# Kernel optimization log

Measured on AMD Instinct MI355X. Metric: run time of the kernel, lower is better.

Reference implementation:

```python
import jax, jax.numpy as jnp
import numpy as np

V = 33279   # num_tokens
E = 256     # embedding_size
H = 512     # hidden_size
NH = 8      # num_heads
L = 4       # num_layers
DH = E // NH
MAXPOS = 64


def _ln(x, g, b):
    mu = jnp.mean(x, axis=-1, keepdims=True)
    var = jnp.mean((x - mu) ** 2, axis=-1, keepdims=True)
    return (x - mu) / jnp.sqrt(var + 1e-5) * g + b


def setup_inputs() -> dict:
    key = jax.random.key(0)
    ks = jax.random.split(key, 32)
    N, S = 128, 64
    label = jax.random.randint(ks[0], (N, S), 0, V)
    # Bernoulli(0.15) BERT-style mask (deterministic stand-in for torch sampling)
    mask = (jax.random.uniform(ks[1], (N, S)) < 0.15).astype(jnp.int32)
    s = 0.02
    inp = {
        'label': label, 'mask': mask,
        'emb': jax.random.normal(ks[2], (V + 1, E)) * s,
        'pos': jax.random.normal(ks[3], (MAXPOS, E)) * s,
        'emb_g': jnp.ones((E,)), 'emb_b': jnp.zeros((E,)),
        # stacked per-layer params (leading dim L)
        'Wq': jax.random.normal(ks[4], (L, E, E)) * s, 'bq': jnp.zeros((L, E)),
        'Wk': jax.random.normal(ks[5], (L, E, E)) * s, 'bk': jnp.zeros((L, E)),
        'Wv': jax.random.normal(ks[6], (L, E, E)) * s, 'bv': jnp.zeros((L, E)),
        'Wo': jax.random.normal(ks[7], (L, E, E)) * s, 'bo': jnp.zeros((L, E)),
        'n1g': jnp.ones((L, E)), 'n1b': jnp.zeros((L, E)),
        'W1': jax.random.normal(ks[8], (L, E, H)) * s, 'b1': jnp.zeros((L, H)),
        'W2': jax.random.normal(ks[9], (L, H, E)) * s, 'b2': jnp.zeros((L, E)),
        'n2g': jnp.ones((L, E)), 'n2b': jnp.zeros((L, E)),
        # decoder head
        'dW1': jax.random.normal(ks[10], (E, E)) * s, 'db1': jnp.zeros((E,)),
        'dng': jnp.ones((E,)), 'dnb': jnp.zeros((E,)),
        'dW2': jax.random.normal(ks[11], (E, V)) * s, 'db2': jnp.zeros((V,)),
    }
    return inp


def reference(label, mask, emb, pos, emb_g, emb_b, Wq, bq, Wk, bk, Wv, bv,
              Wo, bo, n1g, n1b, W1, b1, W2, b2, n2g, n2b,
              dW1, db1, dng, dnb, dW2, db2):
    N, S = label.shape
    src_ids = jnp.where(mask == 1, V, label)  # masked-token id = num_tokens
    # embedding + positional, then LayerNorm (eval: Scaler/Dropout identity)
    x = emb[src_ids] + pos[:S][None, :, :]
    x = _ln(x, emb_g, emb_b)
    temp = jnp.asarray((E // NH) ** 0.5, x.dtype)

    def layer(x, p):
        wq, bq_, wk, bk_, wv, bv_, wo, bo_, g1, b1n, w1, b1_, w2, b2_, g2, b2n = p
        q = (x @ wq + bq_).reshape(N, S, NH, DH).transpose(0, 2, 1, 3)
        k = (x @ wk + bk_).reshape(N, S, NH, DH).transpose(0, 2, 1, 3)
        v = (x @ wv + bv_).reshape(N, S, NH, DH).transpose(0, 2, 1, 3)
        scores = jnp.einsum('nhsd,nhtd->nhst', q, k) / temp
        attn = jax.nn.softmax(scores, axis=-1)
        o = jnp.einsum('nhst,nhtd->nhsd', attn, v)
        o = o.transpose(0, 2, 1, 3).reshape(N, S, E) @ wo + bo_
        x1 = _ln(x + o, g1, b1n)
        ff = jax.nn.gelu(x1 @ w1 + b1_, approximate=False) @ w2 + b2_
        x2 = _ln(x1 + ff, g2, b2n)
        return x2, None

    x, _ = jax.lax.scan(layer, x, (Wq, bq, Wk, bk, Wv, bv, Wo, bo,
                                   n1g, n1b, W1, b1, W2, b2, n2g, n2b))
    # decoder head: linear -> gelu -> LN -> vocab projection
    h = jax.nn.gelu(x @ dW1 + db1, approximate=False)
    h = _ln(h, dng, dnb)
    logits = h @ dW2 + db2               # [N, S, V]
    logp = jax.nn.log_softmax(logits, axis=-1)
    loss = -jnp.take_along_axis(logp, label[..., None], axis=-1).mean()
    score = logits.transpose(0, 2, 1)    # [N, V, S] like torch permute(0,2,1)
    return score, loss
```

## Files before the change

### kernel.cpp

```cpp
#include <hip/hip_runtime.h>
#include <hip/hip_bf16.h>

#define DEVFN static __device__ __forceinline__

constexpr int N_ = 128, S_ = 64, T_ = N_ * S_;
constexpr int E_ = 256, H_ = 512, NH_ = 8, DH_ = 32, L_ = 4;
constexpr int V_ = 33279, VPAD_ = 33280, NVT_ = VPAD_ / 128;

typedef __attribute__((ext_vector_type(8))) short bf16x8;
typedef __attribute__((ext_vector_type(4))) float f32x4;
typedef unsigned short ushort_t;

DEVFN ushort_t f2bf(float f) {
  unsigned int u = __float_as_uint(f);
  unsigned int r = (u + 0x7fffu + ((u >> 16) & 1u)) >> 16;
  return (ushort_t)r;
}
DEVFN float bf2f(ushort_t u) { return __uint_as_float(((unsigned)u) << 16); }

DEVFN float geluf(float x) {
  return 0.5f * x * (1.f + erff(x * 0.70710678118654752440f));
}

DEVFN float wave_sum(float v) {
  #pragma unroll
  for (int off = 32; off >= 1; off >>= 1) v += __shfl_xor(v, off, 64);
  return v;
}

__global__ __launch_bounds__(256) void k_embed_ln(
    const int* __restrict__ label, const int* __restrict__ mask,
    const float* __restrict__ emb, const float* __restrict__ pos,
    const float* __restrict__ g, const float* __restrict__ b,
    float* __restrict__ x, ushort_t* __restrict__ xb) {
  int wv = threadIdx.x >> 6, lane = threadIdx.x & 63;
  int t = blockIdx.x * 4 + wv;
  int s = t & (S_ - 1);
  int id = (mask[t] == 1) ? V_ : label[t];
  int c = lane * 4;
  float4 v = *(const float4*)&emb[(size_t)id * E_ + c];
  float4 p = *(const float4*)&pos[s * E_ + c];
  v.x += p.x; v.y += p.y; v.z += p.z; v.w += p.w;
  float mean = wave_sum(v.x + v.y + v.z + v.w) * (1.f / E_);
  float4 d = {v.x - mean, v.y - mean, v.z - mean, v.w - mean};
  float var = wave_sum(d.x * d.x + d.y * d.y + d.z * d.z + d.w * d.w) * (1.f / E_);
  float rstd = 1.f / sqrtf(var + 1e-5f);
  float4 g4 = *(const float4*)&g[c];
  float4 b4 = *(const float4*)&b[c];
  float4 y = {d.x * rstd * g4.x + b4.x, d.y * rstd * g4.y + b4.y,
              d.z * rstd * g4.z + b4.z, d.w * rstd * g4.w + b4.w};
  *(float4*)&x[(size_t)t * E_ + c] = y;
  ushort4 yb = {f2bf(y.x), f2bf(y.y), f2bf(y.z), f2bf(y.w)};
  *(ushort4*)&xb[(size_t)t * E_ + c] = yb;
}

__global__ __launch_bounds__(256) void k_add_ln(
    const float* __restrict__ a, const float* __restrict__ bsrc,
    const float* __restrict__ g, const float* __restrict__ bet,
    float* __restrict__ y, ushort_t* __restrict__ yb) {
  int wv = threadIdx.x >> 6, lane = threadIdx.x & 63;
  int t = blockIdx.x * 4 + wv;
  int c = lane * 4;
  float4 v = *(const float4*)&a[(size_t)t * E_ + c];
  if (bsrc) {
    float4 u = *(const float4*)&bsrc[(size_t)t * E_ + c];
    v.x += u.x; v.y += u.y; v.z += u.z; v.w += u.w;
  }
  float mean = wave_sum(v.x + v.y + v.z + v.w) * (1.f / E_);
  float4 d = {v.x - mean, v.y - mean, v.z - mean, v.w - mean};
  float var = wave_sum(d.x * d.x + d.y * d.y + d.z * d.z + d.w * d.w) * (1.f / E_);
  float rstd = 1.f / sqrtf(var + 1e-5f);
  float4 g4 = *(const float4*)&g[c];
  float4 b4 = *(const float4*)&bet[c];
  float4 o = {d.x * rstd * g4.x + b4.x, d.y * rstd * g4.y + b4.y,
              d.z * rstd * g4.z + b4.z, d.w * rstd * g4.w + b4.w};
  if (y) *(float4*)&y[(size_t)t * E_ + c] = o;
  if (yb) {
    ushort4 ob = {f2bf(o.x), f2bf(o.y), f2bf(o.z), f2bf(o.w)};
    *(ushort4*)&yb[(size_t)t * E_ + c] = ob;
  }
}

__global__ __launch_bounds__(256) void k_bcat(
    const float* __restrict__ bq, const float* __restrict__ bk,
    const float* __restrict__ bv, float* __restrict__ bqkv) {
  int l = blockIdx.x, i = threadIdx.x;
  bqkv[l * 768 + i]       = bq[l * 256 + i];
  bqkv[l * 768 + 256 + i] = bk[l * 256 + i];
  bqkv[l * 768 + 512 + i] = bv[l * 256 + i];
}

__global__ __launch_bounds__(256) void k_wt(const float* __restrict__ src,
                                            ushort_t* __restrict__ dst,
                                            int K, int J, int dstLayerStride) {
  __shared__ float tile[32][33];
  int j0 = blockIdx.x * 32, k0 = blockIdx.y * 32, l = blockIdx.z;
  src += (size_t)l * K * J;
  dst += (size_t)l * dstLayerStride;
  int tx = threadIdx.x & 31, ty = threadIdx.x >> 5;
  #pragma unroll
  for (int rr = 0; rr < 4; rr++) {
    int kk = ty * 4 + rr;
    tile[kk][tx] = src[(size_t)(k0 + kk) * J + j0 + tx];
  }
  __syncthreads();
  #pragma unroll
  for (int rr = 0; rr < 4; rr++) {
    int jj = ty * 4 + rr;
    dst[(size_t)(j0 + jj) * K + k0 + tx] = f2bf(tile[tx][jj]);
  }
}

template <int K, int OUT_BF16, int GELU_>
__global__ __launch_bounds__(256) void k_mm(
    const ushort_t* __restrict__ Xb, const ushort_t* __restrict__ WT,
    const float* __restrict__ bias, void* __restrict__ C, int Nout) {
  constexpr int STR = K + 8;
  __shared__ ushort_t xs[64 * STR];
  int tid = threadIdx.x, lane = tid & 63, wv = tid >> 6;
  int t0 = blockIdx.x * 64, j0 = blockIdx.y * 64;
  const ushort_t* xsrc = Xb + (size_t)t0 * K;
  for (int i = tid; i < 64 * (K / 8); i += 256) {
    int r = i / (K / 8), c = (i % (K / 8)) * 8;
    *(uint4*)&xs[r * STR + c] = *(const uint4*)&xsrc[(size_t)r * K + c];
  }
  __syncthreads();
  int l15 = lane & 15, l4 = lane >> 4;
  f32x4 acc[4] = {};
  const ushort_t* xrow = &xs[(wv * 16 + l15) * STR + l4 * 8];
  const ushort_t* wrow = WT + (size_t)j0 * K + l4 * 8;
  #pragma unroll
  for (int kb = 0; kb < K / 32; kb++) {
    bf16x8 a = *(const bf16x8*)(xrow + kb * 32);
    #pragma unroll
    for (int st = 0; st < 4; st++) {
      bf16x8 bfr = *(const bf16x8*)(wrow + (size_t)(st * 16 + l15) * K + kb * 32);
      acc[st] = __builtin_amdgcn_mfma_f32_16x16x32_bf16(a, bfr, acc[st], 0, 0, 0);
    }
  }
  #pragma unroll
  for (int st = 0; st < 4; st++) {
    int j = j0 + st * 16 + l15;
    float bv_ = bias[j];
    #pragma unroll
    for (int r = 0; r < 4; r++) {
      float val = acc[st][r] + bv_;
      if (GELU_) val = geluf(val);
      int t = t0 + wv * 16 + l4 * 4 + r;
      if (OUT_BF16)
        ((ushort_t*)C)[(size_t)t * Nout + j] = f2bf(val);
      else
        ((float*)C)[(size_t)t * Nout + j] = val;
    }
  }
}

__global__ __launch_bounds__(256) void k_attn(
    const ushort_t* __restrict__ qkv, ushort_t* __restrict__ o) {
  __shared__ __align__(16) ushort_t vt_[32 * 72];
  __shared__ __align__(16) ushort_t ps[64 * 72];
  int n = blockIdx.x >> 3, h = blockIdx.x & 7;
  int tid = threadIdx.x, lane = tid & 63, wv = tid >> 6;
  int l15 = lane & 15, l4 = lane >> 4;
  const ushort_t* qbase = qkv + (size_t)n * S_ * 768 + h * DH_;
  for (int i = tid; i < S_ * DH_; i += 256) {
    int t = i >> 5, d = i & 31;
    vt_[d * 72 + t] = qbase[(size_t)t * 768 + 512 + d];
  }
  int srow = wv * 16 + l15;
  bf16x8 aq = *(const bf16x8*)&qbase[(size_t)srow * 768 + l4 * 8];
  f32x4 sc[4];
  #pragma unroll
  for (int st = 0; st < 4; st++) {
    bf16x8 bk_ = *(const bf16x8*)&qbase[(size_t)(st * 16 + l15) * 768 + 256 + l4 * 8];
    f32x4 z = {};
    sc[st] = __builtin_amdgcn_mfma_f32_16x16x32_bf16(aq, bk_, z, 0, 0, 0);
  }
  const float scale = 0.17677669529663687f;
  #pragma unroll
  for (int st = 0; st < 4; st++)
    #pragma unroll
    for (int r = 0; r < 4; r++) sc[st][r] *= scale;
  #pragma unroll
  for (int r = 0; r < 4; r++) {
    float m = fmaxf(fmaxf(sc[0][r], sc[1][r]), fmaxf(sc[2][r], sc[3][r]));
    m = fmaxf(m, __shfl_xor(m, 1, 64));
    m = fmaxf(m, __shfl_xor(m, 2, 64));
    m = fmaxf(m, __shfl_xor(m, 4, 64));
    m = fmaxf(m, __shfl_xor(m, 8, 64));
    float p0 = __expf(sc[0][r] - m), p1 = __expf(sc[1][r] - m);
    float p2 = __expf(sc[2][r] - m), p3 = __expf(sc[3][r] - m);
    float sum = p0 + p1 + p2 + p3;
    sum += __shfl_xor(sum, 1, 64);
    sum += __shfl_xor(sum, 2, 64);
    sum += __shfl_xor(sum, 4, 64);
    sum += __shfl_xor(sum, 8, 64);
    float inv = 1.f / sum;
    int prow = (wv * 16 + l4 * 4 + r) * 72;
    ps[prow + 0 * 16 + l15] = f2bf(p0 * inv);
    ps[prow + 1 * 16 + l15] = f2bf(p1 * inv);
    ps[prow + 2 * 16 + l15] = f2bf(p2 * inv);
    ps[prow + 3 * 16 + l15] = f2bf(p3 * inv);
  }
  __syncthreads();
  f32x4 oc[2] = {};
  #pragma unroll
  for (int kb = 0; kb < 2; kb++) {
    bf16x8 ap = *(const bf16x8*)&ps[srow * 72 + kb * 32 + l4 * 8];
    #pragma unroll
    for (int st2 = 0; st2 < 2; st2++) {
      bf16x8 bv_ = *(const bf16x8*)&vt_[(st2 * 16 + l15) * 72 + kb * 32 + l4 * 8];
      oc[st2] = __builtin_amdgcn_mfma_f32_16x16x32_bf16(ap, bv_, oc[st2], 0, 0, 0);
    }
  }
  ushort_t* ob = o + (size_t)n * S_ * E_ + h * DH_;
  #pragma unroll
  for (int st2 = 0; st2 < 2; st2++)
    #pragma unroll
    for (int r = 0; r < 4; r++)
      ob[(size_t)(wv * 16 + l4 * 4 + r) * E_ + st2 * 16 + l15] = f2bf(oc[st2][r]);
}

__global__ __launch_bounds__(256) void k_w2t(const float* __restrict__ w,
                                             ushort_t* __restrict__ wt) {
  __shared__ float tile[32 * 33];
  int tx = threadIdx.x & 31, ty = threadIdx.x >> 5;
  int v0 = blockIdx.x * 32, k0 = blockIdx.y * 32;
  #pragma unroll
  for (int rr = 0; rr < 4; rr++) {
    int kk = ty * 4 + rr;
    int vv = v0 + tx;
    tile[kk * 33 + tx] = (vv < V_) ? w[(size_t)(k0 + kk) * V_ + vv] : 0.f;
  }
  __syncthreads();
  #pragma unroll
  for (int rr = 0; rr < 4; rr++) {
    int vv = ty * 4 + rr;
    wt[(size_t)(v0 + vv) * E_ + k0 + tx] = f2bf(tile[tx * 33 + vv]);
  }
}

__global__ __launch_bounds__(256) void k_vocab(
    const ushort_t* __restrict__ hbf, const ushort_t* __restrict__ wt,
    const float* __restrict__ db2, float* __restrict__ out,
    float* __restrict__ pmax, float* __restrict__ psum) {
  __shared__ ushort_t hs[64 * 264];
  __shared__ float redm[4][64];
  __shared__ float reds[4][64];
  int n = blockIdx.x, vt = blockIdx.y;
  int tid = threadIdx.x, lane = tid & 63, wv = tid >> 6;
  const ushort_t* hsrc = hbf + (size_t)n * S_ * E_;
  for (int i = tid; i < (S_ * E_) / 8; i += 256) {
    int s = i >> 5, kc = (i & 31) * 8;
    *(uint4*)&hs[s * 264 + kc] = *(const uint4*)&hsrc[s * E_ + kc];
  }
  __syncthreads();
  int l15 = lane & 15, l4 = lane >> 4;
  const ushort_t* Ap0 = wt + (size_t)(vt * 128 + wv * 16 + l15) * E_ + l4 * 8;
  const ushort_t* Ap1 = Ap0 + (size_t)64 * E_;
  f32x4 acc[2][4] = {};
  #pragma unroll
  for (int kb = 0; kb < 8; kb++) {
    bf16x8 a0 = *(const bf16x8*)(Ap0 + kb * 32);
    bf16x8 a1 = *(const bf16x8*)(Ap1 + kb * 32);
    #pragma unroll
    for (int st = 0; st < 4; st++) {
      bf16x8 bfr = *(const bf16x8*)&hs[(st * 16 + l15) * 264 + kb * 32 + l4 * 8];
      acc[0][st] = __builtin_amdgcn_mfma_f32_16x16x32_bf16(a0, bfr, acc[0][st], 0, 0, 0);
      acc[1][st] = __builtin_amdgcn_mfma_f32_16x16x32_bf16(a1, bfr, acc[1][st], 0, 0, 0);
    }
  }
  float vals[2][4][4];
  #pragma unroll
  for (int mt = 0; mt < 2; mt++) {
    #pragma unroll
    for (int j = 0; j < 4; j++) {
      int v = vt * 128 + wv * 16 + mt * 64 + l4 * 4 + j;
      bool valid = v < V_;
      float bias = valid ? db2[v] : 0.f;
      size_t ob = ((size_t)n * V_ + v) * S_;
      #pragma unroll
      for (int st = 0; st < 4; st++) {
        float val = valid ? (acc[mt][st][j] + bias) : -INFINITY;
        vals[mt][st][j] = val;
        if (valid) __builtin_nontemporal_store(val, &out[ob + st * 16 + l15]);
      }
    }
  }
  float lm[4];
  #pragma unroll
  for (int st = 0; st < 4; st++) {
    float m = -INFINITY;
    #pragma unroll
    for (int mt = 0; mt < 2; mt++)
      #pragma unroll
      for (int j = 0; j < 4; j++) m = fmaxf(m, vals[mt][st][j]);
    m = fmaxf(m, __shfl_xor(m, 16, 64));
    m = fmaxf(m, __shfl_xor(m, 32, 64));
    lm[st] = m;
  }
  if (l4 == 0) {
    #pragma unroll
    for (int st = 0; st < 4; st++) redm[wv][st * 16 + l15] = lm[st];
  }
  __syncthreads();
  float bm[4], ls[4];
  #pragma unroll
  for (int st = 0; st < 4; st++) {
    int s = st * 16 + l15;
    bm[st] = fmaxf(fmaxf(redm[0][s], redm[1][s]), fmaxf(redm[2][s], redm[3][s]));
    float sum = 0.f;
    #pragma unroll
    for (int mt = 0; mt < 2; mt++)
      #pragma unroll
      for (int j = 0; j < 4; j++) sum += __expf(vals[mt][st][j] - bm[st]);
    sum += __shfl_xor(sum, 16, 64);
    sum += __shfl_xor(sum, 32, 64);
    ls[st] = sum;
  }
  if (l4 == 0) {
    #pragma unroll
    for (int st = 0; st < 4; st++) reds[wv][st * 16 + l15] = ls[st];
  }
  __syncthreads();
  if (wv == 0 && l4 == 0) {
    #pragma unroll
    for (int st = 0; st < 4; st++) {
      int s = st * 16 + l15;
      float bs = reds[0][s] + reds[1][s] + reds[2][s] + reds[3][s];
      size_t pi = ((size_t)n * NVT_ + vt) * S_ + s;
      pmax[pi] = bm[st];
      psum[pi] = bs;
    }
  }
}

__global__ __launch_bounds__(512) void k_lossf(
    const float* __restrict__ pmax, const float* __restrict__ psum,
    const float* __restrict__ out, const int* __restrict__ label,
    float* __restrict__ partial) {
  __shared__ float sm[512], ssum[512];
  int n = blockIdx.x, tid = threadIdx.x;
  int s = tid & 63, qq = tid >> 6;
  float m = -INFINITY, sum = 0.f;
  for (int vt = qq; vt < NVT_; vt += 8) {
    size_t pi = ((size_t)n * NVT_ + vt) * S_ + s;
    float m2 = pmax[pi], s2 = psum[pi];
    float nm = fmaxf(m, m2);
    sum = sum * __expf(m - nm) + s2 * __expf(m2 - nm);
    m = nm;
  }
  sm[tid] = m; ssum[tid] = sum;
  __syncthreads();
  if (qq == 0) {
    float M = sm[s], Sa = ssum[s];
    #pragma unroll
    for (int p = 1; p < 8; p++) {
      float m2 = sm[p * 64 + s], s2 = ssum[p * 64 + s];
      float nm = fmaxf(M, m2);
      Sa = Sa * __expf(M - nm) + s2 * __expf(m2 - nm);
      M = nm;
    }
    float lse = M + logf(Sa);
    int lab = label[n * S_ + s];
    float lx = out[((size_t)n * V_ + lab) * S_ + s];
    partial[n * S_ + s] = lse - lx;
  }
}

__global__ __launch_bounds__(256) void k_loss2(const float* __restrict__ partial,
                                               float* __restrict__ dst) {
  __shared__ float sbuf[4];
  int tid = threadIdx.x;
  float acc = 0.f;
  for (int i = tid; i < T_; i += 256) acc += partial[i];
  #pragma unroll
  for (int off = 32; off >= 1; off >>= 1) acc += __shfl_xor(acc, off, 64);
  int lane = tid & 63, wid = tid >> 6;
  if (lane == 0) sbuf[wid] = acc;
  __syncthreads();
  if (tid == 0) dst[0] = (sbuf[0] + sbuf[1] + sbuf[2] + sbuf[3]) / (float)T_;
}

extern "C" void kernel_launch(void* const* d_in, const int* in_sizes, int n_in,
                              void* d_out, int out_size, void* d_ws, size_t ws_size,
                              hipStream_t stream) {
  const int*   label = (const int*)d_in[0];
  const int*   mask  = (const int*)d_in[1];
  const float* emb   = (const float*)d_in[2];
  const float* pos   = (const float*)d_in[3];
  const float* emb_g = (const float*)d_in[4];
  const float* emb_b = (const float*)d_in[5];
  const float* Wq  = (const float*)d_in[6];
  const float* bq  = (const float*)d_in[7];
  const float* Wk  = (const float*)d_in[8];
  const float* bk  = (const float*)d_in[9];
  const float* Wv  = (const float*)d_in[10];
  const float* bv  = (const float*)d_in[11];
  const float* Wo  = (const float*)d_in[12];
  const float* bo  = (const float*)d_in[13];
  const float* n1g = (const float*)d_in[14];
  const float* n1b = (const float*)d_in[15];
  const float* W1  = (const float*)d_in[16];
  const float* b1  = (const float*)d_in[17];
  const float* W2  = (const float*)d_in[18];
  const float* b2  = (const float*)d_in[19];
  const float* n2g = (const float*)d_in[20];
  const float* n2b = (const float*)d_in[21];
  const float* dW1 = (const float*)d_in[22];
  const float* db1 = (const float*)d_in[23];
  const float* dng = (const float*)d_in[24];
  const float* dnb = (const float*)d_in[25];
  const float* dW2 = (const float*)d_in[26];
  const float* db2 = (const float*)d_in[27];
  float* out = (float*)d_out;
  (void)in_sizes; (void)n_in; (void)out_size; (void)ws_size;

  char* base = (char*)d_ws;
  size_t off = 0;
  auto alloc = [&](size_t bytes) {
    char* p = base + off;
    off += (bytes + 255) & ~(size_t)255;
    return p;
  };
  float*    x    = (float*)alloc((size_t)T_ * E_ * 4);
  ushort_t* xb   = (ushort_t*)alloc((size_t)T_ * E_ * 2);
  float*    x1   = (float*)alloc((size_t)T_ * E_ * 4);
  ushort_t* x1b  = (ushort_t*)alloc((size_t)T_ * E_ * 2);
  ushort_t* qkv  = (ushort_t*)alloc((size_t)T_ * 768 * 2);
  ushort_t* obuf = (ushort_t*)alloc((size_t)T_ * E_ * 2);
  float*    ftmp = (float*)alloc((size_t)T_ * E_ * 4);
  ushort_t* wqkvT = (ushort_t*)alloc((size_t)L_ * 768 * E_ * 2);
  ushort_t* woT   = (ushort_t*)alloc((size_t)L_ * E_ * E_ * 2);
  ushort_t* w1T   = (ushort_t*)alloc((size_t)L_ * H_ * E_ * 2);
  ushort_t* w2T   = (ushort_t*)alloc((size_t)L_ * E_ * H_ * 2);
  ushort_t* dw1T  = (ushort_t*)alloc((size_t)E_ * E_ * 2);
  ushort_t* wt    = (ushort_t*)alloc((size_t)VPAD_ * E_ * 2);
  float*    bqkv  = (float*)alloc((size_t)L_ * 768 * 4);
  float*    partial = (float*)alloc((size_t)T_ * 4);
  ushort_t* ffh = qkv;
  ushort_t* hbf = obuf;
  float* pmax = x;
  float* psum = pmax + (size_t)N_ * NVT_ * S_;

  k_bcat<<<L_, 256, 0, stream>>>(bq, bk, bv, bqkv);
  k_wt<<<dim3(8, 8, L_), 256, 0, stream>>>(Wq, wqkvT + 0 * 65536, E_, E_, 768 * E_);
  k_wt<<<dim3(8, 8, L_), 256, 0, stream>>>(Wk, wqkvT + 1 * 65536, E_, E_, 768 * E_);
  k_wt<<<dim3(8, 8, L_), 256, 0, stream>>>(Wv, wqkvT + 2 * 65536, E_, E_, 768 * E_);
  k_wt<<<dim3(8, 8, L_), 256, 0, stream>>>(Wo, woT, E_, E_, E_ * E_);
  k_wt<<<dim3(16, 8, L_), 256, 0, stream>>>(W1, w1T, E_, H_, H_ * E_);
  k_wt<<<dim3(8, 16, L_), 256, 0, stream>>>(W2, w2T, H_, E_, E_ * H_);
  k_wt<<<dim3(8, 8, 1), 256, 0, stream>>>(dW1, dw1T, E_, E_, E_ * E_);
  k_w2t<<<dim3(VPAD_ / 32, E_ / 32), 256, 0, stream>>>(dW2, wt);

  k_embed_ln<<<T_ / 4, 256, 0, stream>>>(label, mask, emb, pos, emb_g, emb_b, x, xb);

  for (int l = 0; l < L_; l++) {
    k_mm<E_, 1, 0><<<dim3(T_ / 64, 12), 256, 0, stream>>>(
        xb, wqkvT + (size_t)l * 768 * E_, bqkv + l * 768, qkv, 768);
    k_attn<<<N_ * NH_, 256, 0, stream>>>(qkv, obuf);
    k_mm<E_, 0, 0><<<dim3(T_ / 64, 4), 256, 0, stream>>>(
        obuf, woT + (size_t)l * E_ * E_, bo + l * E_, ftmp, E_);
    k_add_ln<<<T_ / 4, 256, 0, stream>>>(x, ftmp, n1g + l * E_, n1b + l * E_, x1, x1b);
    k_mm<E_, 1, 1><<<dim3(T_ / 64, 8), 256, 0, stream>>>(
        x1b, w1T + (size_t)l * H_ * E_, b1 + l * H_, ffh, H_);
    k_mm<H_, 0, 0><<<dim3(T_ / 64, 4), 256, 0, stream>>>(
        ffh, w2T + (size_t)l * E_ * H_, b2 + l * E_, ftmp, E_);
    k_add_ln<<<T_ / 4, 256, 0, stream>>>(x1, ftmp, n2g + l * E_, n2b + l * E_, x, xb);
  }

  k_mm<E_, 0, 1><<<dim3(T_ / 64, 4), 256, 0, stream>>>(xb, dw1T, db1, ftmp, E_);
  k_add_ln<<<T_ / 4, 256, 0, stream>>>(ftmp, nullptr, dng, dnb, nullptr, hbf);

  k_vocab<<<dim3(N_, NVT_), 256, 0, stream>>>(hbf, wt, db2, out, pmax, psum);

  k_lossf<<<N_, 512, 0, stream>>>(pmax, psum, out, label, partial);
  k_loss2<<<1, 256, 0, stream>>>(partial, out + (size_t)N_ * V_ * S_);
}
```

Measured before the change: 946.5 us.

## Fuse attention with output projection and layernorm; fuse FFN2 and decoder matmuls with LN

Replaces the per-head attention kernel, the Wo matmul and the add+LN kernel with one kernel per sequence that runs all heads, projects through Wo from LDS and applies residual plus layernorm in registers. The W2 matmul and the decoder dW1 matmul get a full-row (256-column) fused matmul+LN kernel, and several weight-transpose launches are merged. This removes fp32 intermediate round-trips and many launches, but attention now runs on only 128 blocks with large LDS use and serial heads, so occupancy and parallelism drop.

```diff
diff --git a/kernel.cpp b/kernel.cpp
--- a/kernel.cpp
+++ b/kernel.cpp
@@ -25,6 +25,14 @@
 DEVFN float wave_sum(float v) {
   #pragma unroll
   for (int off = 32; off >= 1; off >>= 1) v += __shfl_xor(v, off, 64);
+  return v;
+}
+
+DEVFN float l15_sum(float v) {
+  v += __shfl_xor(v, 1, 64);
+  v += __shfl_xor(v, 2, 64);
+  v += __shfl_xor(v, 4, 64);
+  v += __shfl_xor(v, 8, 64);
   return v;
 }
 
@@ -54,33 +62,6 @@
   *(ushort4*)&xb[(size_t)t * E_ + c] = yb;
 }
 
-__global__ __launch_bounds__(256) void k_add_ln(
-    const float* __restrict__ a, const float* __restrict__ bsrc,
-    const float* __restrict__ g, const float* __restrict__ bet,
-    float* __restrict__ y, ushort_t* __restrict__ yb) {
-  int wv = threadIdx.x >> 6, lane = threadIdx.x & 63;
-  int t = blockIdx.x * 4 + wv;
-  int c = lane * 4;
-  float4 v = *(const float4*)&a[(size_t)t * E_ + c];
-  if (bsrc) {
-    float4 u = *(const float4*)&bsrc[(size_t)t * E_ + c];
-    v.x += u.x; v.y += u.y; v.z += u.z; v.w += u.w;
-  }
-  float mean = wave_sum(v.x + v.y + v.z + v.w) * (1.f / E_);
-  float4 d = {v.x - mean, v.y - mean, v.z - mean, v.w - mean};
-  float var = wave_sum(d.x * d.x + d.y * d.y + d.z * d.z + d.w * d.w) * (1.f / E_);
-  float rstd = 1.f / sqrtf(var + 1e-5f);
-  float4 g4 = *(const float4*)&g[c];
-  float4 b4 = *(const float4*)&bet[c];
-  float4 o = {d.x * rstd * g4.x + b4.x, d.y * rstd * g4.y + b4.y,
-              d.z * rstd * g4.z + b4.z, d.w * rstd * g4.w + b4.w};
-  if (y) *(float4*)&y[(size_t)t * E_ + c] = o;
-  if (yb) {
-    ushort4 ob = {f2bf(o.x), f2bf(o.y), f2bf(o.z), f2bf(o.w)};
-    *(ushort4*)&yb[(size_t)t * E_ + c] = ob;
-  }
-}
-
 __global__ __launch_bounds__(256) void k_bcat(
     const float* __restrict__ bq, const float* __restrict__ bk,
     const float* __restrict__ bv, float* __restrict__ bqkv) {
@@ -108,6 +89,39 @@
   for (int rr = 0; rr < 4; rr++) {
     int jj = ty * 4 + rr;
     dst[(size_t)(j0 + jj) * K + k0 + tx] = f2bf(tile[tx][jj]);
+  }
+}
+
+__global__ __launch_bounds__(256) void k_wtE(
+    const float* __restrict__ Wq, const float* __restrict__ Wk,
+    const float* __restrict__ Wv, const float* __restrict__ Wo,
+    const float* __restrict__ dW1, ushort_t* __restrict__ wqkvT,
+    ushort_t* __restrict__ woT, ushort_t* __restrict__ dw1T) {
+  __shared__ float tile[32][33];
+  int z = blockIdx.z;
+  const float* src;
+  ushort_t* dst;
+  if (z == 4 * L_) {
+    src = dW1; dst = dw1T;
+  } else {
+    int w = z >> 2, l = z & 3;
+    const float* ws = (w == 0) ? Wq : (w == 1) ? Wk : (w == 2) ? Wv : Wo;
+    src = ws + (size_t)l * E_ * E_;
+    dst = (w < 3) ? (wqkvT + (size_t)l * 768 * E_ + (size_t)w * 256 * E_)
+                  : (woT + (size_t)l * E_ * E_);
+  }
+  int j0 = blockIdx.x * 32, k0 = blockIdx.y * 32;
+  int tx = threadIdx.x & 31, ty = threadIdx.x >> 5;
+  #pragma unroll
+  for (int rr = 0; rr < 4; rr++) {
+    int kk = ty * 4 + rr;
+    tile[kk][tx] = src[(size_t)(k0 + kk) * E_ + j0 + tx];
+  }
+  __syncthreads();
+  #pragma unroll
+  for (int rr = 0; rr < 4; rr++) {
+    int jj = ty * 4 + rr;
+    dst[(size_t)(j0 + jj) * E_ + k0 + tx] = f2bf(tile[tx][jj]);
   }
 }
 
@@ -155,70 +169,222 @@
   }
 }
 
-__global__ __launch_bounds__(256) void k_attn(
-    const ushort_t* __restrict__ qkv, ushort_t* __restrict__ o) {
-  __shared__ __align__(16) ushort_t vt_[32 * 72];
+__global__ __launch_bounds__(256) void k_awl(
+    const ushort_t* __restrict__ qkv, const ushort_t* __restrict__ woT_l,
+    const float* __restrict__ bo_l, const float* __restrict__ xres,
+    const float* __restrict__ g, const float* __restrict__ bet,
+    float* __restrict__ y, ushort_t* __restrict__ yb) {
+  __shared__ __align__(16) ushort_t vt_[NH_ * 32 * 72];
   __shared__ __align__(16) ushort_t ps[64 * 72];
-  int n = blockIdx.x >> 3, h = blockIdx.x & 7;
+  __shared__ __align__(16) ushort_t ol[64 * 264];
+  int n = blockIdx.x;
   int tid = threadIdx.x, lane = tid & 63, wv = tid >> 6;
   int l15 = lane & 15, l4 = lane >> 4;
-  const ushort_t* qbase = qkv + (size_t)n * S_ * 768 + h * DH_;
-  for (int i = tid; i < S_ * DH_; i += 256) {
-    int t = i >> 5, d = i & 31;
-    vt_[d * 72 + t] = qbase[(size_t)t * 768 + 512 + d];
-  }
+  const ushort_t* qb = qkv + (size_t)n * S_ * 768;
+  for (int i = tid; i < 64 * 256; i += 256) {
+    int t = i >> 8, c = i & 255;
+    vt_[c * 72 + t] = qb[(size_t)t * 768 + 512 + c];
+  }
+  __syncthreads();
   int srow = wv * 16 + l15;
-  bf16x8 aq = *(const bf16x8*)&qbase[(size_t)srow * 768 + l4 * 8];
-  f32x4 sc[4];
-  #pragma unroll
-  for (int st = 0; st < 4; st++) {
-    bf16x8 bk_ = *(const bf16x8*)&qbase[(size_t)(st * 16 + l15) * 768 + 256 + l4 * 8];
-    f32x4 z = {};
-    sc[st] = __builtin_amdgcn_mfma_f32_16x16x32_bf16(aq, bk_, z, 0, 0, 0);
-  }
   const float scale = 0.17677669529663687f;
-  #pragma unroll
-  for (int st = 0; st < 4; st++)
-    #pragma unroll
-    for (int r = 0; r < 4; r++) sc[st][r] *= scale;
-  #pragma unroll
-  for (int r = 0; r < 4; r++) {
-    float m = fmaxf(fmaxf(sc[0][r], sc[1][r]), fmaxf(sc[2][r], sc[3][r]));
-    m = fmaxf(m, __shfl_xor(m, 1, 64));
-    m = fmaxf(m, __shfl_xor(m, 2, 64));
-    m = fmaxf(m, __shfl_xor(m, 4, 64));
-    m = fmaxf(m, __shfl_xor(m, 8, 64));
-    float p0 = __expf(sc[0][r] - m), p1 = __expf(sc[1][r] - m);
-    float p2 = __expf(sc[2][r] - m), p3 = __expf(sc[3][r] - m);
-    float sum = p0 + p1 + p2 + p3;
-    sum += __shfl_xor(sum, 1, 64);
-    sum += __shfl_xor(sum, 2, 64);
-    sum += __shfl_xor(sum, 4, 64);
-    sum += __shfl_xor(sum, 8, 64);
-    float inv = 1.f / sum;
-    int prow = (wv * 16 + l4 * 4 + r) * 72;
-    ps[prow + 0 * 16 + l15] = f2bf(p0 * inv);
-    ps[prow + 1 * 16 + l15] = f2bf(p1 * inv);
-    ps[prow + 2 * 16 + l15] = f2bf(p2 * inv);
-    ps[prow + 3 * 16 + l15] = f2bf(p3 * inv);
-  }
-  __syncthreads();
-  f32x4 oc[2] = {};
-  #pragma unroll
-  for (int kb = 0; kb < 2; kb++) {
-    bf16x8 ap = *(const bf16x8*)&ps[srow * 72 + kb * 32 + l4 * 8];
-    #pragma unroll
-    for (int st2 = 0; st2 < 2; st2++) {
-      bf16x8 bv_ = *(const bf16x8*)&vt_[(st2 * 16 + l15) * 72 + kb * 32 + l4 * 8];
-      oc[st2] = __builtin_amdgcn_mfma_f32_16x16x32_bf16(ap, bv_, oc[st2], 0, 0, 0);
-    }
-  }
-  ushort_t* ob = o + (size_t)n * S_ * E_ + h * DH_;
-  #pragma unroll
-  for (int st2 = 0; st2 < 2; st2++)
-    #pragma unroll
-    for (int r = 0; r < 4; r++)
-      ob[(size_t)(wv * 16 + l4 * 4 + r) * E_ + st2 * 16 + l15] = f2bf(oc[st2][r]);
+  for (int h = 0; h < NH_; h++) {
+    const ushort_t* qh = qb + h * DH_;
+    bf16x8 aq = *(const bf16x8*)&qh[(size_t)srow * 768 + l4 * 8];
+    f32x4 sc[4];
+    #pragma unroll
+    for (int st = 0; st < 4; st++) {
+      bf16x8 bk_ = *(const bf16x8*)&qh[(size_t)(st * 16 + l15) * 768 + 256 + l4 * 8];
+      f32x4 z = {};
+      sc[st] = __builtin_amdgcn_mfma_f32_16x16x32_bf16(aq, bk_, z, 0, 0, 0);
+    }
+    #pragma unroll
+    for (int st = 0; st < 4; st++)
+      #pragma unroll
+      for (int r = 0; r < 4; r++) sc[st][r] *= scale;
+    #pragma unroll
+    for (int r = 0; r < 4; r++) {
+      float m = fmaxf(fmaxf(sc[0][r], sc[1][r]), fmaxf(sc[2][r], sc[3][r]));
+      m = fmaxf(m, __shfl_xor(m, 1, 64));
+      m = fmaxf(m, __shfl_xor(m, 2, 64));
+      m = fmaxf(m, __shfl_xor(m, 4, 64));
+      m = fmaxf(m, __shfl_xor(m, 8, 64));
+      float p0 = __expf(sc[0][r] - m), p1 = __expf(sc[1][r] - m);
+      float p2 = __expf(sc[2][r] - m), p3 = __expf(sc[3][r] - m);
+      float sum = p0 + p1 + p2 + p3;
+      sum += __shfl_xor(sum, 1, 64);
+      sum += __shfl_xor(sum, 2, 64);
+      sum += __shfl_xor(sum, 4, 64);
+      sum += __shfl_xor(sum, 8, 64);
+      float inv = 1.f / sum;
+      int prow = (wv * 16 + l4 * 4 + r) * 72;
+      ps[prow + 0 * 16 + l15] = f2bf(p0 * inv);
+      ps[prow + 1 * 16 + l15] = f2bf(p1 * inv);
+      ps[prow + 2 * 16 + l15] = f2bf(p2 * inv);
+      ps[prow + 3 * 16 + l15] = f2bf(p3 * inv);
+    }
+    f32x4 oc[2] = {};
+    #pragma unroll
+    for (int kb = 0; kb < 2; kb++) {
+      bf16x8 ap = *(const bf16x8*)&ps[srow * 72 + kb * 32 + l4 * 8];
+      #pragma unroll
+      for (int st2 = 0; st2 < 2; st2++) {
+        bf16x8 bv_ = *(const bf16x8*)&vt_[(h * 32 + st2 * 16 + l15) * 72 + kb * 32 + l4 * 8];
+        oc[st2] = __builtin_amdgcn_mfma_f32_16x16x32_bf16(ap, bv_, oc[st2], 0, 0, 0);
+      }
+    }
+    #pragma unroll
+    for (int st2 = 0; st2 < 2; st2++)
+      #pragma unroll
+      for (int r = 0; r < 4; r++)
+        ol[(wv * 16 + l4 * 4 + r) * 264 + h * 32 + st2 * 16 + l15] = f2bf(oc[st2][r]);
+  }
+  f32x4 acc[4][4] = {};
+  #pragma unroll
+  for (int kb = 0; kb < 8; kb++) {
+    bf16x8 a = *(const bf16x8*)&ol[(wv * 16 + l15) * 264 + kb * 32 + l4 * 8];
+    #pragma unroll
+    for (int jt = 0; jt < 4; jt++)
+      #pragma unroll
+      for (int st = 0; st < 4; st++) {
+        bf16x8 b = *(const bf16x8*)&woT_l[(size_t)(jt * 64 + st * 16 + l15) * E_ + kb * 32 + l4 * 8];
+        acc[jt][st] = __builtin_amdgcn_mfma_f32_16x16x32_bf16(a, b, acc[jt][st], 0, 0, 0);
+      }
+  }
+  int t0 = n * 64;
+  #pragma unroll
+  for (int jt = 0; jt < 4; jt++)
+    #pragma unroll
+    for (int st = 0; st < 4; st++) {
+      int j = jt * 64 + st * 16 + l15;
+      float bv_ = bo_l[j];
+      #pragma unroll
+      for (int r = 0; r < 4; r++) {
+        int t = t0 + wv * 16 + l4 * 4 + r;
+        acc[jt][st][r] += bv_ + xres[(size_t)t * E_ + j];
+      }
+    }
+  float rsum[4] = {0.f, 0.f, 0.f, 0.f};
+  #pragma unroll
+  for (int jt = 0; jt < 4; jt++)
+    #pragma unroll
+    for (int st = 0; st < 4; st++)
+      #pragma unroll
+      for (int r = 0; r < 4; r++) rsum[r] += acc[jt][st][r];
+  float mean[4], rstd[4];
+  #pragma unroll
+  for (int r = 0; r < 4; r++) mean[r] = l15_sum(rsum[r]) * (1.f / E_);
+  float rvar[4] = {0.f, 0.f, 0.f, 0.f};
+  #pragma unroll
+  for (int jt = 0; jt < 4; jt++)
+    #pragma unroll
+    for (int st = 0; st < 4; st++)
+      #pragma unroll
+      for (int r = 0; r < 4; r++) {
+        float d = acc[jt][st][r] - mean[r];
+        rvar[r] += d * d;
+      }
+  #pragma unroll
+  for (int r = 0; r < 4; r++)
+    rstd[r] = 1.f / sqrtf(l15_sum(rvar[r]) * (1.f / E_) + 1e-5f);
+  #pragma unroll
+  for (int jt = 0; jt < 4; jt++)
+    #pragma unroll
+    for (int st = 0; st < 4; st++) {
+      int j = jt * 64 + st * 16 + l15;
+      float gj = g[j], bj = bet[j];
+      #pragma unroll
+      for (int r = 0; r < 4; r++) {
+        int t = t0 + wv * 16 + l4 * 4 + r;
+        float o = (acc[jt][st][r] - mean[r]) * rstd[r] * gj + bj;
+        y[(size_t)t * E_ + j] = o;
+        yb[(size_t)t * E_ + j] = f2bf(o);
+      }
+    }
+}
+
+template <int K, int GELU_PRE, int HAS_RES, int OUT_F32>
+__global__ __launch_bounds__(128) void k_mm_ln(
+    const ushort_t* __restrict__ Xb, const ushort_t* __restrict__ WT,
+    const float* __restrict__ bias, const float* __restrict__ res,
+    const float* __restrict__ g, const float* __restrict__ bet,
+    float* __restrict__ y, ushort_t* __restrict__ yb) {
+  constexpr int STR = K + 8;
+  __shared__ ushort_t xs[32 * STR];
+  int tid = threadIdx.x, lane = tid & 63, wv = tid >> 6;
+  int t0 = blockIdx.x * 32;
+  const ushort_t* xsrc = Xb + (size_t)t0 * K;
+  for (int i = tid; i < 32 * (K / 8); i += 128) {
+    int r = i / (K / 8), c = (i % (K / 8)) * 8;
+    *(uint4*)&xs[r * STR + c] = *(const uint4*)&xsrc[(size_t)r * K + c];
+  }
+  __syncthreads();
+  int l15 = lane & 15, l4 = lane >> 4;
+  f32x4 acc[4][4] = {};
+  const ushort_t* xrow = &xs[(wv * 16 + l15) * STR + l4 * 8];
+  #pragma unroll
+  for (int kb = 0; kb < K / 32; kb++) {
+    bf16x8 a = *(const bf16x8*)(xrow + kb * 32);
+    #pragma unroll
+    for (int jt = 0; jt < 4; jt++)
+      #pragma unroll
+      for (int st = 0; st < 4; st++) {
+        bf16x8 b = *(const bf16x8*)(WT + (size_t)(jt * 64 + st * 16 + l15) * K + kb * 32 + l4 * 8);
+        acc[jt][st] = __builtin_amdgcn_mfma_f32_16x16x32_bf16(a, b, acc[jt][st], 0, 0, 0);
+      }
+  }
+  #pragma unroll
+  for (int jt = 0; jt < 4; jt++)
+    #pragma unroll
+    for (int st = 0; st < 4; st++) {
+      int j = jt * 64 + st * 16 + l15;
+      float bv_ = bias[j];
+      #pragma unroll
+      for (int r = 0; r < 4; r++) {
+        int t = t0 + wv * 16 + l4 * 4 + r;
+        float v = acc[jt][st][r] + bv_;
+        if (GELU_PRE) v = geluf(v);
+        if (HAS_RES) v += res[(size_t)t * E_ + j];
+        acc[jt][st][r] = v;
+      }
+    }
+  float rsum[4] = {0.f, 0.f, 0.f, 0.f};
+  #pragma unroll
+  for (int jt = 0; jt < 4; jt++)
+    #pragma unroll
+    for (int st = 0; st < 4; st++)
+      #pragma unroll
+      for (int r = 0; r < 4; r++) rsum[r] += acc[jt][st][r];
+  float mean[4], rstd[4];
+  #pragma unroll
+  for (int r = 0; r < 4; r++) mean[r] = l15_sum(rsum[r]) * (1.f / E_);
+  float rvar[4] = {0.f, 0.f, 0.f, 0.f};
+  #pragma unroll
+  for (int jt = 0; jt < 4; jt++)
+    #pragma unroll
+    for (int st = 0; st < 4; st++)
+      #pragma unroll
+      for (int r = 0; r < 4; r++) {
+        float d = acc[jt][st][r] - mean[r];
+        rvar[r] += d * d;
+      }
+  #pragma unroll
+  for (int r = 0; r < 4; r++)
+    rstd[r] = 1.f / sqrtf(l15_sum(rvar[r]) * (1.f / E_) + 1e-5f);
+  #pragma unroll
+  for (int jt = 0; jt < 4; jt++)
+    #pragma unroll
+    for (int st = 0; st < 4; st++) {
+      int j = jt * 64 + st * 16 + l15;
+      float gj = g[j], bj = bet[j];
+      #pragma unroll
+      for (int r = 0; r < 4; r++) {
+        int t = t0 + wv * 16 + l4 * 4 + r;
+        float o = (acc[jt][st][r] - mean[r]) * rstd[r] * gj + bj;
+        if (OUT_F32) y[(size_t)t * E_ + j] = o;
+        yb[(size_t)t * E_ + j] = f2bf(o);
+      }
+    }
 }
 
 __global__ __launch_bounds__(256) void k_w2t(const float* __restrict__ w,
@@ -428,8 +594,7 @@
   float*    x1   = (float*)alloc((size_t)T_ * E_ * 4);
   ushort_t* x1b  = (ushort_t*)alloc((size_t)T_ * E_ * 2);
   ushort_t* qkv  = (ushort_t*)alloc((size_t)T_ * 768 * 2);
-  ushort_t* obuf = (ushort_t*)alloc((size_t)T_ * E_ * 2);
-  float*    ftmp = (float*)alloc((size_t)T_ * E_ * 4);
+  ushort_t* hbf  = (ushort_t*)alloc((size_t)T_ * E_ * 2);
   ushort_t* wqkvT = (ushort_t*)alloc((size_t)L_ * 768 * E_ * 2);
   ushort_t* woT   = (ushort_t*)alloc((size_t)L_ * E_ * E_ * 2);
   ushort_t* w1T   = (ushort_t*)alloc((size_t)L_ * H_ * E_ * 2);
@@ -439,18 +604,13 @@
   float*    bqkv  = (float*)alloc((size_t)L_ * 768 * 4);
   float*    partial = (float*)alloc((size_t)T_ * 4);
   ushort_t* ffh = qkv;
-  ushort_t* hbf = obuf;
   float* pmax = x;
   float* psum = pmax + (size_t)N_ * NVT_ * S_;
 
   k_bcat<<<L_, 256, 0, stream>>>(bq, bk, bv, bqkv);
-  k_wt<<<dim3(8, 8, L_), 256, 0, stream>>>(Wq, wqkvT + 0 * 65536, E_, E_, 768 * E_);
-  k_wt<<<dim3(8, 8, L_), 256, 0, stream>>>(Wk, wqkvT + 1 * 65536, E_, E_, 768 * E_);
-  k_wt<<<dim3(8, 8, L_), 256, 0, stream>>>(Wv, wqkvT + 2 * 65536, E_, E_, 768 * E_);
-  k_wt<<<dim3(8, 8, L_), 256, 0, stream>>>(Wo, woT, E_, E_, E_ * E_);
+  k_wtE<<<dim3(8, 8, 4 * L_ + 1), 256, 0, stream>>>(Wq, Wk, Wv, Wo, dW1, wqkvT, woT, dw1T);
   k_wt<<<dim3(16, 8, L_), 256, 0, stream>>>(W1, w1T, E_, H_, H_ * E_);
   k_wt<<<dim3(8, 16, L_), 256, 0, stream>>>(W2, w2T, H_, E_, E_ * H_);
-  k_wt<<<dim3(8, 8, 1), 256, 0, stream>>>(dW1, dw1T, E_, E_, E_ * E_);
   k_w2t<<<dim3(VPAD_ / 32, E_ / 32), 256, 0, stream>>>(dW2, wt);
 
   k_embed_ln<<<T_ / 4, 256, 0, stream>>>(label, mask, emb, pos, emb_g, emb_b, x, xb);
@@ -458,19 +618,18 @@
   for (int l = 0; l < L_; l++) {
     k_mm<E_, 1, 0><<<dim3(T_ / 64, 12), 256, 0, stream>>>(
         xb, wqkvT + (size_t)l * 768 * E_, bqkv + l * 768, qkv, 768);
-    k_attn<<<N_ * NH_, 256, 0, stream>>>(qkv, obuf);
-    k_mm<E_, 0, 0><<<dim3(T_ / 64, 4), 256, 0, stream>>>(
-        obuf, woT + (size_t)l * E_ * E_, bo + l * E_, ftmp, E_);
-    k_add_ln<<<T_ / 4, 256, 0, stream>>>(x, ftmp, n1g + l * E_, n1b + l * E_, x1, x1b);
+    k_awl<<<N_, 256, 0, stream>>>(
+        qkv, woT + (size_t)l * E_ * E_, bo + l * E_, x,
+        n1g + l * E_, n1b + l * E_, x1, x1b);
     k_mm<E_, 1, 1><<<dim3(T_ / 64, 8), 256, 0, stream>>>(
         x1b, w1T + (size_t)l * H_ * E_, b1 + l * H_, ffh, H_);
-    k_mm<H_, 0, 0><<<dim3(T_ / 64, 4), 256, 0, stream>>>(
-        ffh, w2T + (size_t)l * E_ * H_, b2 + l * E_, ftmp, E_);
-    k_add_ln<<<T_ / 4, 256, 0, stream>>>(x1, ftmp, n2g + l * E_, n2b + l * E_, x, xb);
-  }
-
-  k_mm<E_, 0, 1><<<dim3(T_ / 64, 4), 256, 0, stream>>>(xb, dw1T, db1, ftmp, E_);
-  k_add_ln<<<T_ / 4, 256, 0, stream>>>(ftmp, nullptr, dng, dnb, nullptr, hbf);
+    k_mm_ln<H_, 0, 1, 1><<<T_ / 32, 128, 0, stream>>>(
+        ffh, w2T + (size_t)l * E_ * H_, b2 + l * E_, x1,
+        n2g + l * E_, n2b + l * E_, x, xb);
+  }
+
+  k_mm_ln<E_, 1, 0, 0><<<T_ / 32, 128, 0, stream>>>(
+      xb, dw1T, db1, nullptr, dng, dnb, nullptr, hbf);
 
   k_vocab<<<dim3(N_, NVT_), 256, 0, stream>>>(hbf, wt, db2, out, pmax, psum);
 
```

Result: slower. 1.195 ms (+26.2%).

## Widen vocab tile to 256 rows with online softmax and merge weight transposes

Applied to the files above, without the earlier changes.

The vocab projection kernel now processes 256 vocabulary rows per block in two 128-row halves. The staged hidden tile in shared memory is reused for both halves, and a running max/sum merges their softmax statistics. This halves the number of blocks and the partial max/sum entries the loss kernel must combine, cutting repeated LDS staging of the hidden states. Separately, five small weight-transpose launches are fused into one kernel indexed by blockIdx.z, reducing launch overhead. Fewer blocks may lower occupancy or latency hiding in the vocab kernel.

```diff
diff --git a/kernel.cpp b/kernel.cpp
--- a/kernel.cpp
+++ b/kernel.cpp
@@ -5,7 +5,7 @@
 
 constexpr int N_ = 128, S_ = 64, T_ = N_ * S_;
 constexpr int E_ = 256, H_ = 512, NH_ = 8, DH_ = 32, L_ = 4;
-constexpr int V_ = 33279, VPAD_ = 33280, NVT_ = VPAD_ / 128;
+constexpr int V_ = 33279, VPAD_ = 33280, NVT_ = VPAD_ / 256;
 
 typedef __attribute__((ext_vector_type(8))) short bf16x8;
 typedef __attribute__((ext_vector_type(4))) float f32x4;
@@ -111,6 +111,39 @@
   }
 }
 
+__global__ __launch_bounds__(256) void k_wtE(
+    const float* __restrict__ Wq, const float* __restrict__ Wk,
+    const float* __restrict__ Wv, const float* __restrict__ Wo,
+    const float* __restrict__ dW1, ushort_t* __restrict__ wqkvT,
+    ushort_t* __restrict__ woT, ushort_t* __restrict__ dw1T) {
+  __shared__ float tile[32][33];
+  int z = blockIdx.z;
+  const float* src;
+  ushort_t* dst;
+  if (z == 4 * L_) {
+    src = dW1; dst = dw1T;
+  } else {
+    int w = z >> 2, l = z & 3;
+    const float* ws = (w == 0) ? Wq : (w == 1) ? Wk : (w == 2) ? Wv : Wo;
+    src = ws + (size_t)l * E_ * E_;
+    dst = (w < 3) ? (wqkvT + (size_t)l * 768 * E_ + (size_t)w * 256 * E_)
+                  : (woT + (size_t)l * E_ * E_);
+  }
+  int j0 = blockIdx.x * 32, k0 = blockIdx.y * 32;
+  int tx = threadIdx.x & 31, ty = threadIdx.x >> 5;
+  #pragma unroll
+  for (int rr = 0; rr < 4; rr++) {
+    int kk = ty * 4 + rr;
+    tile[kk][tx] = src[(size_t)(k0 + kk) * E_ + j0 + tx];
+  }
+  __syncthreads();
+  #pragma unroll
+  for (int rr = 0; rr < 4; rr++) {
+    int jj = ty * 4 + rr;
+    dst[(size_t)(j0 + jj) * E_ + k0 + tx] = f2bf(tile[tx][jj]);
+  }
+}
+
 template <int K, int OUT_BF16, int GELU_>
 __global__ __launch_bounds__(256) void k_mm(
     const ushort_t* __restrict__ Xb, const ushort_t* __restrict__ WT,
@@ -256,81 +289,84 @@
   }
   __syncthreads();
   int l15 = lane & 15, l4 = lane >> 4;
-  const ushort_t* Ap0 = wt + (size_t)(vt * 128 + wv * 16 + l15) * E_ + l4 * 8;
-  const ushort_t* Ap1 = Ap0 + (size_t)64 * E_;
-  f32x4 acc[2][4] = {};
-  #pragma unroll
-  for (int kb = 0; kb < 8; kb++) {
-    bf16x8 a0 = *(const bf16x8*)(Ap0 + kb * 32);
-    bf16x8 a1 = *(const bf16x8*)(Ap1 + kb * 32);
-    #pragma unroll
-    for (int st = 0; st < 4; st++) {
-      bf16x8 bfr = *(const bf16x8*)&hs[(st * 16 + l15) * 264 + kb * 32 + l4 * 8];
-      acc[0][st] = __builtin_amdgcn_mfma_f32_16x16x32_bf16(a0, bfr, acc[0][st], 0, 0, 0);
-      acc[1][st] = __builtin_amdgcn_mfma_f32_16x16x32_bf16(a1, bfr, acc[1][st], 0, 0, 0);
-    }
-  }
-  float vals[2][4][4];
-  #pragma unroll
-  for (int mt = 0; mt < 2; mt++) {
-    #pragma unroll
-    for (int j = 0; j < 4; j++) {
-      int v = vt * 128 + wv * 16 + mt * 64 + l4 * 4 + j;
-      bool valid = v < V_;
-      float bias = valid ? db2[v] : 0.f;
-      size_t ob = ((size_t)n * V_ + v) * S_;
+  float rm[4], rs[4];
+  #pragma unroll
+  for (int st = 0; st < 4; st++) { rm[st] = -INFINITY; rs[st] = 0.f; }
+  #pragma unroll
+  for (int h2 = 0; h2 < 2; h2++) {
+    const ushort_t* Ap0 =
+        wt + (size_t)(vt * 256 + h2 * 128 + wv * 16 + l15) * E_ + l4 * 8;
+    const ushort_t* Ap1 = Ap0 + (size_t)64 * E_;
+    f32x4 acc[2][4] = {};
+    #pragma unroll
+    for (int kb = 0; kb < 8; kb++) {
+      bf16x8 a0 = *(const bf16x8*)(Ap0 + kb * 32);
+      bf16x8 a1 = *(const bf16x8*)(Ap1 + kb * 32);
       #pragma unroll
       for (int st = 0; st < 4; st++) {
-        float val = valid ? (acc[mt][st][j] + bias) : -INFINITY;
-        vals[mt][st][j] = val;
-        if (valid) __builtin_nontemporal_store(val, &out[ob + st * 16 + l15]);
+        bf16x8 bfr = *(const bf16x8*)&hs[(st * 16 + l15) * 264 + kb * 32 + l4 * 8];
+        acc[0][st] = __builtin_amdgcn_mfma_f32_16x16x32_bf16(a0, bfr, acc[0][st], 0, 0, 0);
+        acc[1][st] = __builtin_amdgcn_mfma_f32_16x16x32_bf16(a1, bfr, acc[1][st], 0, 0, 0);
       }
     }
-  }
-  float lm[4];
-  #pragma unroll
-  for (int st = 0; st < 4; st++) {
-    float m = -INFINITY;
-    #pragma unroll
-    for (int mt = 0; mt < 2; mt++)
+    float vals[2][4][4];
+    #pragma unroll
+    for (int mt = 0; mt < 2; mt++) {
       #pragma unroll
-      for (int j = 0; j < 4; j++) m = fmaxf(m, vals[mt][st][j]);
-    m = fmaxf(m, __shfl_xor(m, 16, 64));
-    m = fmaxf(m, __shfl_xor(m, 32, 64));
-    lm[st] = m;
+      for (int j = 0; j < 4; j++) {
+        int v = vt * 256 + h2 * 128 + wv * 16 + mt * 64 + l4 * 4 + j;
+        bool valid = v < V_;
+        float bias = valid ? db2[v] : 0.f;
+        size_t ob = ((size_t)n * V_ + v) * S_;
+        #pragma unroll
+        for (int st = 0; st < 4; st++) {
+          float val = valid ? (acc[mt][st][j] + bias) : -INFINITY;
+          vals[mt][st][j] = val;
+          if (valid) __builtin_nontemporal_store(val, &out[ob + st * 16 + l15]);
+        }
+      }
+    }
+    #pragma unroll
+    for (int st = 0; st < 4; st++) {
+      float m = -INFINITY;
+      #pragma unroll
+      for (int mt = 0; mt < 2; mt++)
+        #pragma unroll
+        for (int j = 0; j < 4; j++) m = fmaxf(m, vals[mt][st][j]);
+      m = fmaxf(m, __shfl_xor(m, 16, 64));
+      m = fmaxf(m, __shfl_xor(m, 32, 64));
+      float sum = 0.f;
+      #pragma unroll
+      for (int mt = 0; mt < 2; mt++)
+        #pragma unroll
+        for (int j = 0; j < 4; j++) sum += __expf(vals[mt][st][j] - m);
+      sum += __shfl_xor(sum, 16, 64);
+      sum += __shfl_xor(sum, 32, 64);
+      float nm = fmaxf(rm[st], m);
+      rs[st] = rs[st] * __expf(rm[st] - nm) + sum * __expf(m - nm);
+      rm[st] = nm;
+    }
   }
   if (l4 == 0) {
     #pragma unroll
-    for (int st = 0; st < 4; st++) redm[wv][st * 16 + l15] = lm[st];
-  }
-  __syncthreads();
-  float bm[4], ls[4];
-  #pragma unroll
-  for (int st = 0; st < 4; st++) {
-    int s = st * 16 + l15;
-    bm[st] = fmaxf(fmaxf(redm[0][s], redm[1][s]), fmaxf(redm[2][s], redm[3][s]));
-    float sum = 0.f;
-    #pragma unroll
-    for (int mt = 0; mt < 2; mt++)
-      #pragma unroll
-      for (int j = 0; j < 4; j++) sum += __expf(vals[mt][st][j] - bm[st]);
-    sum += __shfl_xor(sum, 16, 64);
-    sum += __shfl_xor(sum, 32, 64);
-    ls[st] = sum;
-  }
-  if (l4 == 0) {
-    #pragma unroll
-    for (int st = 0; st < 4; st++) reds[wv][st * 16 + l15] = ls[st];
+    for (int st = 0; st < 4; st++) {
+      redm[wv][st * 16 + l15] = rm[st];
+      reds[wv][st * 16 + l15] = rs[st];
+    }
   }
   __syncthreads();
   if (wv == 0 && l4 == 0) {
     #pragma unroll
     for (int st = 0; st < 4; st++) {
       int s = st * 16 + l15;
-      float bs = reds[0][s] + reds[1][s] + reds[2][s] + reds[3][s];
+      float M = fmaxf(fmaxf(redm[0][s], redm[1][s]), fmaxf(redm[2][s], redm[3][s]));
+      float Sa = reds[0][s] * __expf(redm[0][s] - M) +
+                 reds[1][s] * __expf(redm[1][s] - M) +
+                 reds[2][s] * __expf(redm[2][s] - M) +
+                 reds[3][s] * __expf(redm[3][s] - M);
       size_t pi = ((size_t)n * NVT_ + vt) * S_ + s;
-      pmax[pi] = bm[st];
-      psum[pi] = bs;
+      pmax[pi] = M;
+      psum[pi] = Sa;
     }
   }
 }
@@ -444,13 +480,9 @@
   float* psum = pmax + (size_t)N_ * NVT_ * S_;
 
   k_bcat<<<L_, 256, 0, stream>>>(bq, bk, bv, bqkv);
-  k_wt<<<dim3(8, 8, L_), 256, 0, stream>>>(Wq, wqkvT + 0 * 65536, E_, E_, 768 * E_);
-  k_wt<<<dim3(8, 8, L_), 256, 0, stream>>>(Wk, wqkvT + 1 * 65536, E_, E_, 768 * E_);
-  k_wt<<<dim3(8, 8, L_), 256, 0, stream>>>(Wv, wqkvT + 2 * 65536, E_, E_, 768 * E_);
-  k_wt<<<dim3(8, 8, L_), 256, 0, stream>>>(Wo, woT, E_, E_, E_ * E_);
+  k_wtE<<<dim3(8, 8, 4 * L_ + 1), 256, 0, stream>>>(Wq, Wk, Wv, Wo, dW1, wqkvT, woT, dw1T);
   k_wt<<<dim3(16, 8, L_), 256, 0, stream>>>(W1, w1T, E_, H_, H_ * E_);
   k_wt<<<dim3(8, 16, L_), 256, 0, stream>>>(W2, w2T, H_, E_, E_ * H_);
-  k_wt<<<dim3(8, 8, 1), 256, 0, stream>>>(dW1, dw1T, E_, E_, E_ * E_);
   k_w2t<<<dim3(VPAD_ / 32, E_ / 32), 256, 0, stream>>>(dW2, wt);
 
   k_embed_ln<<<T_ / 4, 256, 0, stream>>>(label, mask, emb, pos, emb_g, emb_b, x, xb);
```

Result: faster. 923.0 us (-2.5%).
